# Optimization experiments

Hardware: AMD Instinct MI355X
Metric: run time of the kernel (lower is better)

## Reference

```python
import jax, jax.numpy as jnp
import numpy as np

EMB_DIM = 1024
ATTN_DIM = 1024


def setup_inputs() -> dict:
    key = jax.random.key(0)
    k_x, k_wk, k_wq, k_wv = jax.random.split(key, 4)
    bound = 1.0 / np.sqrt(EMB_DIM)  # nn.Linear default init range
    return {
        "embedded": jax.random.normal(k_x, (4, 2048, EMB_DIM), dtype=jnp.float32),
        "W_k": jax.random.uniform(k_wk, (ATTN_DIM, EMB_DIM), jnp.float32, -bound, bound),
        "W_q": jax.random.uniform(k_wq, (ATTN_DIM, EMB_DIM), jnp.float32, -bound, bound),
        "W_v": jax.random.uniform(k_wv, (ATTN_DIM, EMB_DIM), jnp.float32, -bound, bound),
    }


def reference(embedded, W_k, W_q, W_v):
    # Linear (bias=False): y = x @ W.T
    K = jnp.einsum("bse,ae->bsa", embedded, W_k)
    Q = jnp.einsum("bse,ae->bsa", embedded, W_q)
    V = jnp.einsum("bse,ae->bsa", embedded, W_v)
    S = K.shape[1]
    scale = 1.0 / jnp.sqrt(jnp.float32(ATTN_DIM))
    scores = jnp.einsum("bqa,bka->bqk", Q, K) * scale  # [B, S, S]
    causal = jnp.tril(jnp.ones((S, S), dtype=bool))  # True = keep
    scores = jnp.where(causal[None, :, :], scores, -jnp.inf)
    attn = jax.nn.softmax(scores, axis=2)
    out = jnp.einsum("bqk,bka->bqa", attn, V)
    # torch.round(x, decimals=4)
    return jnp.round(out * 1e4) / 1e4
```

## Files before the change

### kernel.cpp

```cpp
#include <hip/hip_runtime.h>
#include <stdint.h>

#define B_ 4
#define S_ 2048
#define E_ 1024
#define D_ 1024

typedef short  bf16x8 __attribute__((ext_vector_type(8)));
typedef float  f32x4  __attribute__((ext_vector_type(4)));

static __device__ __forceinline__ unsigned short f2bf(float f) {
    unsigned int u = __float_as_uint(f);
    u += 0x7fffu + ((u >> 16) & 1u);
    return (unsigned short)(u >> 16);
}

static __device__ __forceinline__ void async16(const unsigned short* g, unsigned short* l) {
    auto gp = (const __attribute__((address_space(1))) void*)(uintptr_t)g;
    auto lp = (__attribute__((address_space(3))) void*)(uintptr_t)l;
    __builtin_amdgcn_global_load_lds(gp, lp, 16, 0, 0);
}

__global__ __launch_bounds__(256)
void convert_kernel(const float* __restrict__ x,  const float* __restrict__ Wk,
                    const float* __restrict__ Wq, const float* __restrict__ Wv,
                    unsigned short* __restrict__ xb, unsigned short* __restrict__ Wb,
                    float* __restrict__ rowsum)
{
    if (blockIdx.x < 8) {
        float4 z = {0.f, 0.f, 0.f, 0.f};
        *(float4*)(rowsum + (size_t)blockIdx.x * 1024 + threadIdx.x * 4) = z;
    }
    const long long idx = ((long long)blockIdx.x * 256 + threadIdx.x) * 4;
    const float* src; unsigned short* dst; long long off;
    if (idx < (long long)B_ * S_ * E_) {
        src = x; dst = xb; off = idx;
    } else {
        long long w = idx - (long long)B_ * S_ * E_;
        const int sel = (int)(w >> 20);
        off = w & 1048575LL;
        src = (sel == 0) ? Wk : (sel == 1) ? Wq : Wv;
        dst = Wb + ((long long)sel << 20);
    }
    const float4 f = *(const float4*)(src + off);
    ushort4 u = { f2bf(f.x), f2bf(f.y), f2bf(f.z), f2bf(f.w) };
    *(ushort4*)(dst + off) = u;
}

__global__ __launch_bounds__(256)
void proj_kernel(const unsigned short* __restrict__ xb,
                 const unsigned short* __restrict__ Wb,
                 unsigned short* __restrict__ Qb,
                 unsigned short* __restrict__ Kb,
                 unsigned short* __restrict__ Vt)
{
    __shared__ __align__(16) unsigned short As[128 * 32];
    __shared__ __align__(16) unsigned short Bs[128 * 32];

    const int t    = threadIdx.x;
    const int m0   = blockIdx.x * 128;
    const int ny   = blockIdx.y;
    const int wsel = ny >> 3;
    const int nloc = (ny & 7) * 128;

    const int lane = t & 63, wave = t >> 6;
    const int l15 = lane & 15, quad = lane >> 4;
    const int wm = wave & 1, wn = wave >> 1;
    const int lr = lane >> 2, lc = (lane & 3) * 8;

    const unsigned short* gA = xb + (size_t)(m0 + wave * 32 + lr) * E_ + lc;
    const unsigned short* gB = Wb + (size_t)(ny * 128 + wave * 32 + lr) * E_ + lc;
    unsigned short* lA = &As[wave * 1024];
    unsigned short* lB = &Bs[wave * 1024];

    f32x4 acc[4][4];
    #pragma unroll
    for (int i = 0; i < 4; i++)
        #pragma unroll
        for (int j = 0; j < 4; j++) acc[i][j] = {0.f, 0.f, 0.f, 0.f};

    for (int k0 = 0; k0 < E_; k0 += 32) {
        __syncthreads();
        async16(gA + k0,            lA);
        async16(gA + k0 + 16 * E_,  lA + 512);
        async16(gB + k0,            lB);
        async16(gB + k0 + 16 * E_,  lB + 512);
        __syncthreads();

        bf16x8 af[4], bfr[4];
        #pragma unroll
        for (int i = 0; i < 4; i++)
            af[i] = *(const bf16x8*)&As[(wm * 64 + i * 16 + l15) * 32 + quad * 8];
        #pragma unroll
        for (int j = 0; j < 4; j++)
            bfr[j] = *(const bf16x8*)&Bs[(wn * 64 + j * 16 + l15) * 32 + quad * 8];
        #pragma unroll
        for (int i = 0; i < 4; i++)
            #pragma unroll
            for (int j = 0; j < 4; j++)
                acc[i][j] = __builtin_amdgcn_mfma_f32_16x16x32_bf16(af[i], bfr[j], acc[i][j], 0, 0, 0);
    }

    if (wsel == 0) {
        #pragma unroll
        for (int i = 0; i < 4; i++)
            #pragma unroll
            for (int j = 0; j < 4; j++) {
                const int gn = nloc + wn * 64 + j * 16 + l15;
                #pragma unroll
                for (int r = 0; r < 4; r++) {
                    const int gm = m0 + wm * 64 + i * 16 + quad * 4 + r;
                    Kb[(size_t)gm * D_ + gn] = f2bf(acc[i][j][r]);
                }
            }
    } else if (wsel == 1) {
        #pragma unroll
        for (int i = 0; i < 4; i++)
            #pragma unroll
            for (int j = 0; j < 4; j++) {
                const int gn = nloc + wn * 64 + j * 16 + l15;
                #pragma unroll
                for (int r = 0; r < 4; r++) {
                    const int gm = m0 + wm * 64 + i * 16 + quad * 4 + r;
                    Qb[(size_t)gm * D_ + gn] = f2bf(acc[i][j][r] * 0.03125f);
                }
            }
    } else {
        #pragma unroll
        for (int i = 0; i < 4; i++)
            #pragma unroll
            for (int j = 0; j < 4; j++) {
                const int s0 = m0 + wm * 64 + i * 16 + quad * 4;
                const int b  = s0 >> 11, sl = s0 & (S_ - 1);
                const int gn = nloc + wn * 64 + j * 16 + l15;
                ushort4 u = { f2bf(acc[i][j][0]), f2bf(acc[i][j][1]),
                              f2bf(acc[i][j][2]), f2bf(acc[i][j][3]) };
                *(ushort4*)&Vt[((size_t)(b << 10) + gn) * S_ + sl] = u;
            }
    }
}

__global__ __launch_bounds__(256)
void expscores_kernel(const unsigned short* __restrict__ Qb,
                      const unsigned short* __restrict__ Kb,
                      unsigned short* __restrict__ P,
                      float* __restrict__ rowsum)
{
    const int tl = blockIdx.x, b = blockIdx.y;
    int mt = (int)((sqrtf(8.0f * tl + 1.0f) - 1.0f) * 0.5f);
    while ((mt + 1) * (mt + 2) / 2 <= tl) mt++;
    while (mt * (mt + 1) / 2 > tl) mt--;
    const int nt = tl - mt * (mt + 1) / 2;

    __shared__ __align__(16) unsigned short As[128 * 32];
    __shared__ __align__(16) unsigned short Bs[128 * 32];

    const int t = threadIdx.x;
    const int m0 = mt * 128, n0 = nt * 128;

    const int lane = t & 63, wave = t >> 6;
    const int l15 = lane & 15, quad = lane >> 4;
    const int wm = wave & 1, wn = wave >> 1;
    const int lr = lane >> 2, lc = (lane & 3) * 8;

    const unsigned short* gA = Qb + (size_t)b * S_ * D_ + (size_t)(m0 + wave * 32 + lr) * D_ + lc;
    const unsigned short* gB = Kb + (size_t)b * S_ * D_ + (size_t)(n0 + wave * 32 + lr) * D_ + lc;
    unsigned short* lA = &As[wave * 1024];
    unsigned short* lB = &Bs[wave * 1024];

    f32x4 acc[4][4];
    #pragma unroll
    for (int i = 0; i < 4; i++)
        #pragma unroll
        for (int j = 0; j < 4; j++) acc[i][j] = {0.f, 0.f, 0.f, 0.f};

    for (int k0 = 0; k0 < D_; k0 += 32) {
        __syncthreads();
        async16(gA + k0,            lA);
        async16(gA + k0 + 16 * D_,  lA + 512);
        async16(gB + k0,            lB);
        async16(gB + k0 + 16 * D_,  lB + 512);
        __syncthreads();

        bf16x8 af[4], bfr[4];
        #pragma unroll
        for (int i = 0; i < 4; i++)
            af[i] = *(const bf16x8*)&As[(wm * 64 + i * 16 + l15) * 32 + quad * 8];
        #pragma unroll
        for (int j = 0; j < 4; j++)
            bfr[j] = *(const bf16x8*)&Bs[(wn * 64 + j * 16 + l15) * 32 + quad * 8];
        #pragma unroll
        for (int i = 0; i < 4; i++)
            #pragma unroll
            for (int j = 0; j < 4; j++)
                acc[i][j] = __builtin_amdgcn_mfma_f32_16x16x32_bf16(af[i], bfr[j], acc[i][j], 0, 0, 0);
    }

    unsigned short* Pb = P + (size_t)b * S_ * S_;
    #pragma unroll
    for (int i = 0; i < 4; i++)
        #pragma unroll
        for (int j = 0; j < 4; j++) {
            const int gn = n0 + wn * 64 + j * 16 + l15;
            #pragma unroll
            for (int r = 0; r < 4; r++) {
                const int gm = m0 + wm * 64 + i * 16 + quad * 4 + r;
                const float e = (gn <= gm) ? __expf(acc[i][j][r]) : 0.f;
                acc[i][j][r] = e;
                Pb[(size_t)gm * S_ + gn] = f2bf(e);
            }
        }

    float* rs = rowsum + (size_t)b * S_;
    #pragma unroll
    for (int i = 0; i < 4; i++) {
        float rsub[4];
        #pragma unroll
        for (int r = 0; r < 4; r++) {
            float s = acc[i][0][r] + acc[i][1][r] + acc[i][2][r] + acc[i][3][r];
            #pragma unroll
            for (int off = 8; off; off >>= 1) s += __shfl_xor(s, off);
            rsub[r] = s;
        }
        if (l15 == 0) {
            #pragma unroll
            for (int r = 0; r < 4; r++) {
                const int gm = m0 + wm * 64 + i * 16 + quad * 4 + r;
                atomicAdd(&rs[gm], rsub[r]);
            }
        }
    }
}

__global__ __launch_bounds__(256)
void pv_kernel(const unsigned short* __restrict__ P,
               const unsigned short* __restrict__ Vt,
               const float* __restrict__ rowsum,
               float* __restrict__ out)
{
    const int mt = 15 - blockIdx.x;
    const int nt = blockIdx.y, b = blockIdx.z;

    __shared__ __align__(16) unsigned short As[128 * 32];
    __shared__ __align__(16) unsigned short Bs[128 * 32];

    const int t = threadIdx.x;
    const int m0 = mt * 128, n0 = nt * 128;
    const int kend = m0 + 128;

    const int lane = t & 63, wave = t >> 6;
    const int l15 = lane & 15, quad = lane >> 4;
    const int wm = wave & 1, wn = wave >> 1;
    const int lr = lane >> 2, lc = (lane & 3) * 8;

    const unsigned short* gA = P  + (size_t)b * S_ * S_ + (size_t)(m0 + wave * 32 + lr) * S_ + lc;
    const unsigned short* gB = Vt + (size_t)b * D_ * S_ + (size_t)(n0 + wave * 32 + lr) * S_ + lc;
    unsigned short* lA = &As[wave * 1024];
    unsigned short* lB = &Bs[wave * 1024];

    f32x4 acc[4][4];
    #pragma unroll
    for (int i = 0; i < 4; i++)
        #pragma unroll
        for (int j = 0; j < 4; j++) acc[i][j] = {0.f, 0.f, 0.f, 0.f};

    for (int k0 = 0; k0 < kend; k0 += 32) {
        __syncthreads();
        async16(gA + k0,            lA);
        async16(gA + k0 + 16 * S_,  lA + 512);
        async16(gB + k0,            lB);
        async16(gB + k0 + 16 * S_,  lB + 512);
        __syncthreads();

        bf16x8 af[4], bfr[4];
        #pragma unroll
        for (int i = 0; i < 4; i++)
            af[i] = *(const bf16x8*)&As[(wm * 64 + i * 16 + l15) * 32 + quad * 8];
        #pragma unroll
        for (int j = 0; j < 4; j++)
            bfr[j] = *(const bf16x8*)&Bs[(wn * 64 + j * 16 + l15) * 32 + quad * 8];
        #pragma unroll
        for (int i = 0; i < 4; i++)
            #pragma unroll
            for (int j = 0; j < 4; j++)
                acc[i][j] = __builtin_amdgcn_mfma_f32_16x16x32_bf16(af[i], bfr[j], acc[i][j], 0, 0, 0);
    }

    const float* rs = rowsum + (size_t)b * S_;
    #pragma unroll
    for (int i = 0; i < 4; i++) {
        float inv[4];
        #pragma unroll
        for (int r = 0; r < 4; r++) {
            const int gm = m0 + wm * 64 + i * 16 + quad * 4 + r;
            inv[r] = 1.0f / rs[gm];
        }
        #pragma unroll
        for (int j = 0; j < 4; j++) {
            const int gn = n0 + wn * 64 + j * 16 + l15;
            #pragma unroll
            for (int r = 0; r < 4; r++) {
                const int gm = m0 + wm * 64 + i * 16 + quad * 4 + r;
                out[((size_t)b * S_ + gm) * D_ + gn] = rintf(acc[i][j][r] * inv[r] * 1e4f) * 1e-4f;
            }
        }
    }
}

extern "C" void kernel_launch(void* const* d_in, const int* in_sizes, int n_in,
                              void* d_out, int out_size, void* d_ws, size_t ws_size,
                              hipStream_t stream)
{
    (void)in_sizes; (void)n_in; (void)out_size; (void)ws_size;
    const float* x  = (const float*)d_in[0];
    const float* Wk = (const float*)d_in[1];
    const float* Wq = (const float*)d_in[2];
    const float* Wv = (const float*)d_in[3];
    float* out = (float*)d_out;

    char* ws = (char*)d_ws;
    unsigned short* Qb = (unsigned short*)ws;
    unsigned short* Kb = Qb + (size_t)B_ * S_ * D_;
    unsigned short* Vt = Kb + (size_t)B_ * S_ * D_;
    unsigned short* P  = Vt + (size_t)B_ * D_ * S_;
    unsigned short* xb = P;
    unsigned short* Wb = xb + (size_t)B_ * S_ * E_;
    float* rowsum = (float*)(P + (size_t)B_ * S_ * S_);

    const int conv_blocks = (B_ * S_ * E_ + 3 * D_ * E_) / (256 * 4);
    convert_kernel  <<<conv_blocks, 256, 0, stream>>>(x, Wk, Wq, Wv, xb, Wb, rowsum);
    proj_kernel     <<<dim3(64, 24, 1),   256, 0, stream>>>(xb, Wb, Qb, Kb, Vt);
    expscores_kernel<<<dim3(136, B_, 1),  256, 0, stream>>>(Qb, Kb, P, rowsum);
    pv_kernel       <<<dim3(16, 8, B_),   256, 0, stream>>>(P, Vt, rowsum, out);
}
```

Before: 259.2 us.

## Widen K-tile to 64 with XOR-swizzled LDS and replace rowsum atomics with partials

All three GEMM kernels now stage 64-wide K slices into LDS using an XOR swizzle on the column chunk. This halves the number of barrier pairs per K loop and is meant to avoid LDS bank conflicts on the fragment reads. The softmax row-sum atomics are replaced by per-column-tile partial sums written to a buffer, which pv_kernel reduces itself and broadcasts with a shuffle. That also removes the zeroing of the row sums in the convert kernel. The changes double LDS per block and add launch_bounds occupancy hints, and pv_kernel now does a small extra reduction up front.

New measurement: 232.2 us. 1.12x faster.

```diff
diff --git a/kernel.cpp b/kernel.cpp
--- a/kernel.cpp
+++ b/kernel.cpp
@@ -21,16 +21,12 @@
     __builtin_amdgcn_global_load_lds(gp, lp, 16, 0, 0);
 }
 
+
 __global__ __launch_bounds__(256)
 void convert_kernel(const float* __restrict__ x,  const float* __restrict__ Wk,
                     const float* __restrict__ Wq, const float* __restrict__ Wv,
-                    unsigned short* __restrict__ xb, unsigned short* __restrict__ Wb,
-                    float* __restrict__ rowsum)
-{
-    if (blockIdx.x < 8) {
-        float4 z = {0.f, 0.f, 0.f, 0.f};
-        *(float4*)(rowsum + (size_t)blockIdx.x * 1024 + threadIdx.x * 4) = z;
-    }
+                    unsigned short* __restrict__ xb, unsigned short* __restrict__ Wb)
+{
     const long long idx = ((long long)blockIdx.x * 256 + threadIdx.x) * 4;
     const float* src; unsigned short* dst; long long off;
     if (idx < (long long)B_ * S_ * E_) {
@@ -47,15 +43,15 @@
     *(ushort4*)(dst + off) = u;
 }
 
-__global__ __launch_bounds__(256)
+__global__ __launch_bounds__(256, 4)
 void proj_kernel(const unsigned short* __restrict__ xb,
                  const unsigned short* __restrict__ Wb,
                  unsigned short* __restrict__ Qb,
                  unsigned short* __restrict__ Kb,
                  unsigned short* __restrict__ Vt)
 {
-    __shared__ __align__(16) unsigned short As[128 * 32];
-    __shared__ __align__(16) unsigned short Bs[128 * 32];
+    __shared__ __align__(16) unsigned short As[128 * 64];
+    __shared__ __align__(16) unsigned short Bs[128 * 64];
 
     const int t    = threadIdx.x;
     const int m0   = blockIdx.x * 128;
@@ -66,12 +62,18 @@
     const int lane = t & 63, wave = t >> 6;
     const int l15 = lane & 15, quad = lane >> 4;
     const int wm = wave & 1, wn = wave >> 1;
-    const int lr = lane >> 2, lc = (lane & 3) * 8;
-
-    const unsigned short* gA = xb + (size_t)(m0 + wave * 32 + lr) * E_ + lc;
-    const unsigned short* gB = Wb + (size_t)(ny * 128 + wave * 32 + lr) * E_ + lc;
-    unsigned short* lA = &As[wave * 1024];
-    unsigned short* lB = &Bs[wave * 1024];
+    const int sr = lane >> 3;
+    const int sq = ((lane & 7) ^ sr) * 8;
+    const int l7 = l15 & 7;
+    const int rcA0 = (wm * 64 + l15) * 64 + ((quad ^ l7) * 8);
+    const int rcA1 = (wm * 64 + l15) * 64 + (((4 + quad) ^ l7) * 8);
+    const int rcB0 = (wn * 64 + l15) * 64 + ((quad ^ l7) * 8);
+    const int rcB1 = (wn * 64 + l15) * 64 + (((4 + quad) ^ l7) * 8);
+
+    const unsigned short* gA = xb + (size_t)(m0 + wave * 32 + sr) * E_ + sq;
+    const unsigned short* gB = Wb + (size_t)(ny * 128 + wave * 32 + sr) * E_ + sq;
+    unsigned short* lA = &As[wave * 2048];
+    unsigned short* lB = &Bs[wave * 2048];
 
     f32x4 acc[4][4];
     #pragma unroll
@@ -79,26 +81,29 @@
         #pragma unroll
         for (int j = 0; j < 4; j++) acc[i][j] = {0.f, 0.f, 0.f, 0.f};
 
-    for (int k0 = 0; k0 < E_; k0 += 32) {
-        __syncthreads();
-        async16(gA + k0,            lA);
-        async16(gA + k0 + 16 * E_,  lA + 512);
-        async16(gB + k0,            lB);
-        async16(gB + k0 + 16 * E_,  lB + 512);
-        __syncthreads();
-
-        bf16x8 af[4], bfr[4];
-        #pragma unroll
-        for (int i = 0; i < 4; i++)
-            af[i] = *(const bf16x8*)&As[(wm * 64 + i * 16 + l15) * 32 + quad * 8];
-        #pragma unroll
-        for (int j = 0; j < 4; j++)
-            bfr[j] = *(const bf16x8*)&Bs[(wn * 64 + j * 16 + l15) * 32 + quad * 8];
-        #pragma unroll
-        for (int i = 0; i < 4; i++)
-            #pragma unroll
-            for (int j = 0; j < 4; j++)
-                acc[i][j] = __builtin_amdgcn_mfma_f32_16x16x32_bf16(af[i], bfr[j], acc[i][j], 0, 0, 0);
+    for (int k0 = 0; k0 < E_; k0 += 64) {
+        __syncthreads();
+        #pragma unroll
+        for (int i = 0; i < 4; i++) {
+            async16(gA + k0 + i * 8 * E_, lA + i * 512);
+            async16(gB + k0 + i * 8 * E_, lB + i * 512);
+        }
+        __syncthreads();
+
+        #pragma unroll
+        for (int s = 0; s < 2; s++) {
+            bf16x8 af[4], bfr[4];
+            const int ra = s ? rcA1 : rcA0, rb = s ? rcB1 : rcB0;
+            #pragma unroll
+            for (int i = 0; i < 4; i++) af[i]  = *(const bf16x8*)&As[ra + i * 1024];
+            #pragma unroll
+            for (int j = 0; j < 4; j++) bfr[j] = *(const bf16x8*)&Bs[rb + j * 1024];
+            #pragma unroll
+            for (int i = 0; i < 4; i++)
+                #pragma unroll
+                for (int j = 0; j < 4; j++)
+                    acc[i][j] = __builtin_amdgcn_mfma_f32_16x16x32_bf16(af[i], bfr[j], acc[i][j], 0, 0, 0);
+        }
     }
 
     if (wsel == 0) {
@@ -140,11 +145,11 @@
     }
 }
 
-__global__ __launch_bounds__(256)
+__global__ __launch_bounds__(256, 4)
 void expscores_kernel(const unsigned short* __restrict__ Qb,
                       const unsigned short* __restrict__ Kb,
                       unsigned short* __restrict__ P,
-                      float* __restrict__ rowsum)
+                      float* __restrict__ rowpart)
 {
     const int tl = blockIdx.x, b = blockIdx.y;
     int mt = (int)((sqrtf(8.0f * tl + 1.0f) - 1.0f) * 0.5f);
@@ -152,8 +157,8 @@
     while (mt * (mt + 1) / 2 > tl) mt--;
     const int nt = tl - mt * (mt + 1) / 2;
 
-    __shared__ __align__(16) unsigned short As[128 * 32];
-    __shared__ __align__(16) unsigned short Bs[128 * 32];
+    __shared__ __align__(16) unsigned short As[128 * 64];
+    __shared__ __align__(16) unsigned short Bs[128 * 64];
 
     const int t = threadIdx.x;
     const int m0 = mt * 128, n0 = nt * 128;
@@ -161,12 +166,18 @@
     const int lane = t & 63, wave = t >> 6;
     const int l15 = lane & 15, quad = lane >> 4;
     const int wm = wave & 1, wn = wave >> 1;
-    const int lr = lane >> 2, lc = (lane & 3) * 8;
-
-    const unsigned short* gA = Qb + (size_t)b * S_ * D_ + (size_t)(m0 + wave * 32 + lr) * D_ + lc;
-    const unsigned short* gB = Kb + (size_t)b * S_ * D_ + (size_t)(n0 + wave * 32 + lr) * D_ + lc;
-    unsigned short* lA = &As[wave * 1024];
-    unsigned short* lB = &Bs[wave * 1024];
+    const int sr = lane >> 3;
+    const int sq = ((lane & 7) ^ sr) * 8;
+    const int l7 = l15 & 7;
+    const int rcA0 = (wm * 64 + l15) * 64 + ((quad ^ l7) * 8);
+    const int rcA1 = (wm * 64 + l15) * 64 + (((4 + quad) ^ l7) * 8);
+    const int rcB0 = (wn * 64 + l15) * 64 + ((quad ^ l7) * 8);
+    const int rcB1 = (wn * 64 + l15) * 64 + (((4 + quad) ^ l7) * 8);
+
+    const unsigned short* gA = Qb + (size_t)b * S_ * D_ + (size_t)(m0 + wave * 32 + sr) * D_ + sq;
+    const unsigned short* gB = Kb + (size_t)b * S_ * D_ + (size_t)(n0 + wave * 32 + sr) * D_ + sq;
+    unsigned short* lA = &As[wave * 2048];
+    unsigned short* lB = &Bs[wave * 2048];
 
     f32x4 acc[4][4];
     #pragma unroll
@@ -174,26 +185,29 @@
         #pragma unroll
         for (int j = 0; j < 4; j++) acc[i][j] = {0.f, 0.f, 0.f, 0.f};
 
-    for (int k0 = 0; k0 < D_; k0 += 32) {
-        __syncthreads();
-        async16(gA + k0,            lA);
-        async16(gA + k0 + 16 * D_,  lA + 512);
-        async16(gB + k0,            lB);
-        async16(gB + k0 + 16 * D_,  lB + 512);
-        __syncthreads();
-
-        bf16x8 af[4], bfr[4];
-        #pragma unroll
-        for (int i = 0; i < 4; i++)
-            af[i] = *(const bf16x8*)&As[(wm * 64 + i * 16 + l15) * 32 + quad * 8];
-        #pragma unroll
-        for (int j = 0; j < 4; j++)
-            bfr[j] = *(const bf16x8*)&Bs[(wn * 64 + j * 16 + l15) * 32 + quad * 8];
-        #pragma unroll
-        for (int i = 0; i < 4; i++)
-            #pragma unroll
-            for (int j = 0; j < 4; j++)
-                acc[i][j] = __builtin_amdgcn_mfma_f32_16x16x32_bf16(af[i], bfr[j], acc[i][j], 0, 0, 0);
+    for (int k0 = 0; k0 < D_; k0 += 64) {
+        __syncthreads();
+        #pragma unroll
+        for (int i = 0; i < 4; i++) {
+            async16(gA + k0 + i * 8 * D_, lA + i * 512);
+            async16(gB + k0 + i * 8 * D_, lB + i * 512);
+        }
+        __syncthreads();
+
+        #pragma unroll
+        for (int s = 0; s < 2; s++) {
+            bf16x8 af[4], bfr[4];
+            const int ra = s ? rcA1 : rcA0, rb = s ? rcB1 : rcB0;
+            #pragma unroll
+            for (int i = 0; i < 4; i++) af[i]  = *(const bf16x8*)&As[ra + i * 1024];
+            #pragma unroll
+            for (int j = 0; j < 4; j++) bfr[j] = *(const bf16x8*)&Bs[rb + j * 1024];
+            #pragma unroll
+            for (int i = 0; i < 4; i++)
+                #pragma unroll
+                for (int j = 0; j < 4; j++)
+                    acc[i][j] = __builtin_amdgcn_mfma_f32_16x16x32_bf16(af[i], bfr[j], acc[i][j], 0, 0, 0);
+        }
     }
 
     unsigned short* Pb = P + (size_t)b * S_ * S_;
@@ -211,7 +225,7 @@
             }
         }
 
-    float* rs = rowsum + (size_t)b * S_;
+    float* rp = rowpart + ((size_t)b * 32 + nt * 2 + wn) * S_;
     #pragma unroll
     for (int i = 0; i < 4; i++) {
         float rsub[4];
@@ -224,25 +238,23 @@
         }
         if (l15 == 0) {
             #pragma unroll
-            for (int r = 0; r < 4; r++) {
-                const int gm = m0 + wm * 64 + i * 16 + quad * 4 + r;
-                atomicAdd(&rs[gm], rsub[r]);
-            }
-        }
-    }
-}
-
-__global__ __launch_bounds__(256)
+            for (int r = 0; r < 4; r++)
+                rp[m0 + wm * 64 + i * 16 + quad * 4 + r] = rsub[r];
+        }
+    }
+}
+
+__global__ __launch_bounds__(256, 4)
 void pv_kernel(const unsigned short* __restrict__ P,
                const unsigned short* __restrict__ Vt,
-               const float* __restrict__ rowsum,
+               const float* __restrict__ rowpart,
                float* __restrict__ out)
 {
     const int mt = 15 - blockIdx.x;
     const int nt = blockIdx.y, b = blockIdx.z;
 
-    __shared__ __align__(16) unsigned short As[128 * 32];
-    __shared__ __align__(16) unsigned short Bs[128 * 32];
+    __shared__ __align__(16) unsigned short As[128 * 64];
+    __shared__ __align__(16) unsigned short Bs[128 * 64];
 
     const int t = threadIdx.x;
     const int m0 = mt * 128, n0 = nt * 128;
@@ -251,12 +263,24 @@
     const int lane = t & 63, wave = t >> 6;
     const int l15 = lane & 15, quad = lane >> 4;
     const int wm = wave & 1, wn = wave >> 1;
-    const int lr = lane >> 2, lc = (lane & 3) * 8;
-
-    const unsigned short* gA = P  + (size_t)b * S_ * S_ + (size_t)(m0 + wave * 32 + lr) * S_ + lc;
-    const unsigned short* gB = Vt + (size_t)b * D_ * S_ + (size_t)(n0 + wave * 32 + lr) * S_ + lc;
-    unsigned short* lA = &As[wave * 1024];
-    unsigned short* lB = &Bs[wave * 1024];
+    const int sr = lane >> 3;
+    const int sq = ((lane & 7) ^ sr) * 8;
+    const int l7 = l15 & 7;
+    const int rcA0 = (wm * 64 + l15) * 64 + ((quad ^ l7) * 8);
+    const int rcA1 = (wm * 64 + l15) * 64 + (((4 + quad) ^ l7) * 8);
+    const int rcB0 = (wn * 64 + l15) * 64 + ((quad ^ l7) * 8);
+    const int rcB1 = (wn * 64 + l15) * 64 + (((4 + quad) ^ l7) * 8);
+
+    const int nsl = 2 * mt + 2;
+    const float* rp = rowpart + (size_t)b * 32 * S_ + (m0 + wm * 64 + lane);
+    float rsum = 0.f;
+    for (int k = 0; k < nsl; k++) rsum += rp[(size_t)k * S_];
+    const float invr = 1.0f / rsum;
+
+    const unsigned short* gA = P  + (size_t)b * S_ * S_ + (size_t)(m0 + wave * 32 + sr) * S_ + sq;
+    const unsigned short* gB = Vt + (size_t)b * D_ * S_ + (size_t)(n0 + wave * 32 + sr) * S_ + sq;
+    unsigned short* lA = &As[wave * 2048];
+    unsigned short* lB = &Bs[wave * 2048];
 
     f32x4 acc[4][4];
     #pragma unroll
@@ -264,44 +288,41 @@
         #pragma unroll
         for (int j = 0; j < 4; j++) acc[i][j] = {0.f, 0.f, 0.f, 0.f};
 
-    for (int k0 = 0; k0 < kend; k0 += 32) {
-        __syncthreads();
-        async16(gA + k0,            lA);
-        async16(gA + k0 + 16 * S_,  lA + 512);
-        async16(gB + k0,            lB);
-        async16(gB + k0 + 16 * S_,  lB + 512);
-        __syncthreads();
-
-        bf16x8 af[4], bfr[4];
-        #pragma unroll
-        for (int i = 0; i < 4; i++)
-            af[i] = *(const bf16x8*)&As[(wm * 64 + i * 16 + l15) * 32 + quad * 8];
-        #pragma unroll
-        for (int j = 0; j < 4; j++)
-            bfr[j] = *(const bf16x8*)&Bs[(wn * 64 + j * 16 + l15) * 32 + quad * 8];
-        #pragma unroll
-        for (int i = 0; i < 4; i++)
-            #pragma unroll
-            for (int j = 0; j < 4; j++)
-                acc[i][j] = __builtin_amdgcn_mfma_f32_16x16x32_bf16(af[i], bfr[j], acc[i][j], 0, 0, 0);
-    }
-
-    const float* rs = rowsum + (size_t)b * S_;
+    for (int k0 = 0; k0 < kend; k0 += 64) {
+        __syncthreads();
+        #pragma unroll
+        for (int i = 0; i < 4; i++) {
+            async16(gA + k0 + i * 8 * S_, lA + i * 512);
+            async16(gB + k0 + i * 8 * S_, lB + i * 512);
+        }
+        __syncthreads();
+
+        #pragma unroll
+        for (int s = 0; s < 2; s++) {
+            bf16x8 af[4], bfr[4];
+            const int ra = s ? rcA1 : rcA0, rb = s ? rcB1 : rcB0;
+            #pragma unroll
+            for (int i = 0; i < 4; i++) af[i]  = *(const bf16x8*)&As[ra + i * 1024];
+            #pragma unroll
+            for (int j = 0; j < 4; j++) bfr[j] = *(const bf16x8*)&Bs[rb + j * 1024];
+            #pragma unroll
+            for (int i = 0; i < 4; i++)
+                #pragma unroll
+                for (int j = 0; j < 4; j++)
+                    acc[i][j] = __builtin_amdgcn_mfma_f32_16x16x32_bf16(af[i], bfr[j], acc[i][j], 0, 0, 0);
+        }
+    }
+
     #pragma unroll
     for (int i = 0; i < 4; i++) {
-        float inv[4];
         #pragma unroll
         for (int r = 0; r < 4; r++) {
+            const float vr = __shfl(invr, i * 16 + quad * 4 + r);
             const int gm = m0 + wm * 64 + i * 16 + quad * 4 + r;
-            inv[r] = 1.0f / rs[gm];
-        }
-        #pragma unroll
-        for (int j = 0; j < 4; j++) {
-            const int gn = n0 + wn * 64 + j * 16 + l15;
-            #pragma unroll
-            for (int r = 0; r < 4; r++) {
-                const int gm = m0 + wm * 64 + i * 16 + quad * 4 + r;
-                out[((size_t)b * S_ + gm) * D_ + gn] = rintf(acc[i][j][r] * inv[r] * 1e4f) * 1e-4f;
+            #pragma unroll
+            for (int j = 0; j < 4; j++) {
+                const int gn = n0 + wn * 64 + j * 16 + l15;
+                out[((size_t)b * S_ + gm) * D_ + gn] = rintf(acc[i][j][r] * vr * 1e4f) * 1e-4f;
             }
         }
     }
@@ -325,11 +346,11 @@
     unsigned short* P  = Vt + (size_t)B_ * D_ * S_;
     unsigned short* xb = P;
     unsigned short* Wb = xb + (size_t)B_ * S_ * E_;
-    float* rowsum = (float*)(P + (size_t)B_ * S_ * S_);
+    float* rowpart = (float*)(P + (size_t)B_ * S_ * S_);
 
     const int conv_blocks = (B_ * S_ * E_ + 3 * D_ * E_) / (256 * 4);
-    convert_kernel  <<<conv_blocks, 256, 0, stream>>>(x, Wk, Wq, Wv, xb, Wb, rowsum);
+    convert_kernel  <<<conv_blocks, 256, 0, stream>>>(x, Wk, Wq, Wv, xb, Wb);
     proj_kernel     <<<dim3(64, 24, 1),   256, 0, stream>>>(xb, Wb, Qb, Kb, Vt);
-    expscores_kernel<<<dim3(136, B_, 1),  256, 0, stream>>>(Qb, Kb, P, rowsum);
-    pv_kernel       <<<dim3(16, 8, B_),   256, 0, stream>>>(P, Vt, rowsum, out);
-}
+    expscores_kernel<<<dim3(136, B_, 1),  256, 0, stream>>>(Qb, Kb, P, rowpart);
+    pv_kernel       <<<dim3(16, 8, B_),   256, 0, stream>>>(P, Vt, rowpart, out);
+}
```
